# Kernel tuning notes

Measured on AMD Instinct MI355X. Metric: run time of the kernel, lower is better.

## Reference

```python
import jax, jax.numpy as jnp
import numpy as np

N_NODES = 100000
N_EDGES = 1600000
EMBED_DIM = 64


def setup_inputs() -> dict:
    key = jax.random.key(0)
    k_x, k_e, k_w, k_b = jax.random.split(key, 4)
    x = jax.random.normal(k_x, (N_NODES, EMBED_DIM), dtype=jnp.float32)
    edge_index = jax.random.randint(k_e, (2, N_EDGES), 0, N_NODES, dtype=jnp.int64)
    # nn.Linear(embed_dim, embed_dim): weight [out, in], bias [out]
    W = jax.random.normal(k_w, (EMBED_DIM, EMBED_DIM), dtype=jnp.float32) * (1.0 / np.sqrt(EMBED_DIM))
    b = jax.random.normal(k_b, (EMBED_DIM,), dtype=jnp.float32) * 0.01
    return {"x": x, "edge_index": edge_index, "W": W, "b": b, "num_node": N_NODES}


def reference(x, edge_index, W, b, num_node):
    source_nodes, target_nodes = edge_index[0], edge_index[1]
    # h = relu(Linear(x))  -> [N, d]
    h = jax.nn.relu(jnp.einsum("nd,od->no", x, W) + b)
    # gather messages at target nodes: [E, d]
    msgs = h[target_nodes]
    # scatter-add into source node slots (index_add_)
    aggr = jax.ops.segment_sum(msgs, source_nodes, num_segments=num_node)
    # mean normalization: bincount clamped to >= 1
    counts = jnp.bincount(source_nodes, length=num_node).astype(jnp.float32)
    counts = jnp.maximum(counts, 1.0)
    # dropout is identity at inference (training=False)
    return aggr / counts[:, None]
```

## Files before the change

### kernel.cpp

```cpp
#include <hip/hip_runtime.h>
#include <hip/hip_bf16.h>

#define DIM 64
#define SCAN_B 256

__global__ void detect_layout_kernel(const int* __restrict__ ei32,
                                     int* __restrict__ flag) {
  int v = ei32[2 * threadIdx.x + 1];
  unsigned long long m = __ballot(v != 0);
  if (threadIdx.x == 0) *flag = (m == 0ULL) ? 1 : 0;
}

__device__ __forceinline__ int load_idx(const int* ei32, int is64, size_t pos) {
  return is64 ? ei32[2 * pos] : ei32[pos];
}

__global__ __launch_bounds__(256) void hist_rank_kernel(
    const int* __restrict__ ei32, const int* __restrict__ flag,
    int* __restrict__ counts, int* __restrict__ rank, int E) {
  int e = blockIdx.x * 256 + threadIdx.x;
  if (e >= E) return;
  int src = load_idx(ei32, *flag, (size_t)e);
  rank[e] = atomicAdd(&counts[src], 1);
}

__global__ void scan1_kernel(const int* __restrict__ counts,
                             int* __restrict__ offsets,
                             int* __restrict__ partials, int N) {
  __shared__ int s[SCAN_B];
  int t = threadIdx.x;
  int i = blockIdx.x * SCAN_B + t;
  int v = (i < N) ? counts[i] : 0;
  s[t] = v;
  __syncthreads();
  for (int off = 1; off < SCAN_B; off <<= 1) {
    int add = (t >= off) ? s[t - off] : 0;
    __syncthreads();
    s[t] += add;
    __syncthreads();
  }
  if (i < N) offsets[i] = s[t] - v;
  if (t == SCAN_B - 1) partials[blockIdx.x] = s[t];
}

__global__ void scan2_kernel(int* __restrict__ partials, int nb) {
  __shared__ int s[512];
  int t = threadIdx.x;
  int v = (t < nb) ? partials[t] : 0;
  s[t] = v;
  __syncthreads();
  for (int off = 1; off < 512; off <<= 1) {
    int add = (t >= off) ? s[t - off] : 0;
    __syncthreads();
    s[t] += add;
    __syncthreads();
  }
  if (t < nb) partials[t] = s[t] - v;
}

__global__ void scan3_kernel(int* __restrict__ offsets,
                             const int* __restrict__ partials, int N) {
  int i = blockIdx.x * SCAN_B + threadIdx.x;
  if (i < N) offsets[i] += partials[blockIdx.x];
}

__global__ __launch_bounds__(256) void place_kernel(
    const int* __restrict__ ei32, const int* __restrict__ flag,
    const int* __restrict__ offsets, const int* __restrict__ rank,
    int* __restrict__ bucket, int E) {
  int e = blockIdx.x * 256 + threadIdx.x;
  if (e >= E) return;
  int is64 = *flag;
  int src = load_idx(ei32, is64, (size_t)e);
  int tgt = load_idx(ei32, is64, (size_t)E + e);
  __builtin_nontemporal_store(tgt, &bucket[offsets[src] + rank[e]]);
}

__global__ __launch_bounds__(256) void linear_relu_kernel(
    const float* __restrict__ x, const float* __restrict__ W,
    const float* __restrict__ b, float* __restrict__ h, int N) {
  __shared__ float Ws[DIM * DIM];
  __shared__ float bs[DIM];
  for (int i = threadIdx.x; i < DIM * DIM; i += 256) Ws[i] = W[i];
  if (threadIdx.x < DIM) bs[threadIdx.x] = b[threadIdx.x];
  __syncthreads();

  int row = blockIdx.x * 256 + threadIdx.x;
  if (row >= N) return;

  const float4* xr = (const float4*)(x + (size_t)row * DIM);
  float acc[DIM];
#pragma unroll
  for (int o = 0; o < DIM; ++o) acc[o] = bs[o];

#pragma unroll
  for (int i4 = 0; i4 < DIM / 4; ++i4) {
    float4 xv = xr[i4];
#pragma unroll
    for (int o = 0; o < DIM; ++o) {
      const float* wrow = &Ws[o * DIM + i4 * 4];
      acc[o] = fmaf(xv.x, wrow[0], acc[o]);
      acc[o] = fmaf(xv.y, wrow[1], acc[o]);
      acc[o] = fmaf(xv.z, wrow[2], acc[o]);
      acc[o] = fmaf(xv.w, wrow[3], acc[o]);
    }
  }

  float4* hr = (float4*)(h + (size_t)row * DIM);
#pragma unroll
  for (int o4 = 0; o4 < DIM / 4; ++o4) {
    float4 v;
    v.x = fmaxf(acc[o4 * 4 + 0], 0.0f);
    v.y = fmaxf(acc[o4 * 4 + 1], 0.0f);
    v.z = fmaxf(acc[o4 * 4 + 2], 0.0f);
    v.w = fmaxf(acc[o4 * 4 + 3], 0.0f);
    hr[o4] = v;
  }
}

__global__ __launch_bounds__(256) void gather_kernel(
    const float* __restrict__ h, const int* __restrict__ offsets,
    const int* __restrict__ counts, const int* __restrict__ bucket,
    float* __restrict__ out, int N) {
  int wid = (blockIdx.x * 256 + threadIdx.x) >> 6;
  int lane = threadIdx.x & 63;
  if (wid >= N) return;

  int deg = counts[wid];
  int start = offsets[wid];
  float a0 = 0.0f, a1 = 0.0f, a2 = 0.0f, a3 = 0.0f;

  for (int j0 = 0; j0 < deg; j0 += 64) {
    int m = min(deg - j0, 64);
    int t = (lane < m) ? __builtin_nontemporal_load(&bucket[start + j0 + lane])
                       : 0;
    int j = 0;
    for (; j + 4 <= m; j += 4) {
      int t0 = __shfl(t, j);
      int t1 = __shfl(t, j + 1);
      int t2 = __shfl(t, j + 2);
      int t3 = __shfl(t, j + 3);
      float v0 = h[(size_t)t0 * DIM + lane];
      float v1 = h[(size_t)t1 * DIM + lane];
      float v2 = h[(size_t)t2 * DIM + lane];
      float v3 = h[(size_t)t3 * DIM + lane];
      a0 += v0;
      a1 += v1;
      a2 += v2;
      a3 += v3;
    }
    for (; j < m; ++j) {
      int tj = __shfl(t, j);
      a0 += h[(size_t)tj * DIM + lane];
    }
  }

  float c = (float)max(deg, 1);
  float acc = (a0 + a1) + (a2 + a3);
  __builtin_nontemporal_store(acc / c, &out[(size_t)wid * DIM + lane]);
}

extern "C" void kernel_launch(void* const* d_in, const int* in_sizes, int n_in,
                              void* d_out, int out_size, void* d_ws, size_t ws_size,
                              hipStream_t stream) {
  const float* x = (const float*)d_in[0];
  const int* ei32 = (const int*)d_in[1];
  const float* W = (const float*)d_in[2];
  const float* b = (const float*)d_in[3];

  const int N = in_sizes[0] / DIM;
  const int E = in_sizes[1] / 2;

  float* out = (float*)d_out;

  char* p = (char*)d_ws;
  int* bucket = (int*)p;   p += (size_t)E * 4;
  int* counts = (int*)p;   p += (size_t)N * 4;
  int* offsets = (int*)p;  p += (size_t)N * 4;
  int* partials = (int*)p; p += 512 * 4;
  int* flag = (int*)p;     p += 16;
  p = (char*)(((uintptr_t)p + 15) & ~(uintptr_t)15);
  float* h = (float*)p;
  int* rank = (int*)p;

  const int nb1 = (N + SCAN_B - 1) / SCAN_B;
  const int eb = (E + 255) / 256;

  hipMemsetAsync(counts, 0, (size_t)N * 4, stream);

  detect_layout_kernel<<<1, 64, 0, stream>>>(ei32, flag);

  hist_rank_kernel<<<eb, 256, 0, stream>>>(ei32, flag, counts, rank, E);

  scan1_kernel<<<nb1, SCAN_B, 0, stream>>>(counts, offsets, partials, N);
  scan2_kernel<<<1, 512, 0, stream>>>(partials, nb1);
  scan3_kernel<<<nb1, SCAN_B, 0, stream>>>(offsets, partials, N);

  place_kernel<<<eb, 256, 0, stream>>>(ei32, flag, offsets, rank, bucket, E);

  linear_relu_kernel<<<(N + 255) / 256, 256, 0, stream>>>(x, W, b, h, N);

  gather_kernel<<<(N * 64 + 255) / 256, 256, 0, stream>>>(h, offsets, counts,
                                                          bucket, out, N);
}
```

Before: 330.0 us.

## Fuse linear-relu with histogram kernel and widen gather unroll to eight

Merges the linear+ReLU and the edge histogram/rank pass into one launch, using block-index ranges to split the work. Both can then run concurrently, and one kernel launch is removed. The rank array moves into the output buffer (which gather later overwrites) so it no longer aliases h, and its stores and loads become nontemporal. The gather loop now keeps eight independent loads in flight instead of four. The fused kernel reserves shared memory for every block, including the histogram blocks that never use it, which may lower occupancy for those blocks.

```diff
diff --git a/kernel.cpp b/kernel.cpp
--- a/kernel.cpp
+++ b/kernel.cpp
@@ -15,13 +15,59 @@
   return is64 ? ei32[2 * pos] : ei32[pos];
 }
 
-__global__ __launch_bounds__(256) void hist_rank_kernel(
+__global__ __launch_bounds__(256) void lin_hist_kernel(
+    const float* __restrict__ x, const float* __restrict__ W,
+    const float* __restrict__ b, float* __restrict__ h, int N, int nbLin,
     const int* __restrict__ ei32, const int* __restrict__ flag,
     int* __restrict__ counts, int* __restrict__ rank, int E) {
-  int e = blockIdx.x * 256 + threadIdx.x;
-  if (e >= E) return;
-  int src = load_idx(ei32, *flag, (size_t)e);
-  rank[e] = atomicAdd(&counts[src], 1);
+  __shared__ float Ws[DIM * DIM];
+  __shared__ float bs[DIM];
+
+  if (blockIdx.x >= nbLin) {
+    int e = (blockIdx.x - nbLin) * 256 + threadIdx.x;
+    if (e < E) {
+      int src = load_idx(ei32, *flag, (size_t)e);
+      int r = atomicAdd(&counts[src], 1);
+      __builtin_nontemporal_store(r, &rank[e]);
+    }
+    return;
+  }
+
+  for (int i = threadIdx.x; i < DIM * DIM; i += 256) Ws[i] = W[i];
+  if (threadIdx.x < DIM) bs[threadIdx.x] = b[threadIdx.x];
+  __syncthreads();
+
+  int row = blockIdx.x * 256 + threadIdx.x;
+  if (row >= N) return;
+
+  const float4* xr = (const float4*)(x + (size_t)row * DIM);
+  float acc[DIM];
+#pragma unroll
+  for (int o = 0; o < DIM; ++o) acc[o] = bs[o];
+
+#pragma unroll
+  for (int i4 = 0; i4 < DIM / 4; ++i4) {
+    float4 xv = xr[i4];
+#pragma unroll
+    for (int o = 0; o < DIM; ++o) {
+      const float* wrow = &Ws[o * DIM + i4 * 4];
+      acc[o] = fmaf(xv.x, wrow[0], acc[o]);
+      acc[o] = fmaf(xv.y, wrow[1], acc[o]);
+      acc[o] = fmaf(xv.z, wrow[2], acc[o]);
+      acc[o] = fmaf(xv.w, wrow[3], acc[o]);
+    }
+  }
+
+  float4* hr = (float4*)(h + (size_t)row * DIM);
+#pragma unroll
+  for (int o4 = 0; o4 < DIM / 4; ++o4) {
+    float4 v;
+    v.x = fmaxf(acc[o4 * 4 + 0], 0.0f);
+    v.y = fmaxf(acc[o4 * 4 + 1], 0.0f);
+    v.z = fmaxf(acc[o4 * 4 + 2], 0.0f);
+    v.w = fmaxf(acc[o4 * 4 + 3], 0.0f);
+    hr[o4] = v;
+  }
 }
 
 __global__ void scan1_kernel(const int* __restrict__ counts,
@@ -73,49 +119,8 @@
   int is64 = *flag;
   int src = load_idx(ei32, is64, (size_t)e);
   int tgt = load_idx(ei32, is64, (size_t)E + e);
-  __builtin_nontemporal_store(tgt, &bucket[offsets[src] + rank[e]]);
-}
-
-__global__ __launch_bounds__(256) void linear_relu_kernel(
-    const float* __restrict__ x, const float* __restrict__ W,
-    const float* __restrict__ b, float* __restrict__ h, int N) {
-  __shared__ float Ws[DIM * DIM];
-  __shared__ float bs[DIM];
-  for (int i = threadIdx.x; i < DIM * DIM; i += 256) Ws[i] = W[i];
-  if (threadIdx.x < DIM) bs[threadIdx.x] = b[threadIdx.x];
-  __syncthreads();
-
-  int row = blockIdx.x * 256 + threadIdx.x;
-  if (row >= N) return;
-
-  const float4* xr = (const float4*)(x + (size_t)row * DIM);
-  float acc[DIM];
-#pragma unroll
-  for (int o = 0; o < DIM; ++o) acc[o] = bs[o];
-
-#pragma unroll
-  for (int i4 = 0; i4 < DIM / 4; ++i4) {
-    float4 xv = xr[i4];
-#pragma unroll
-    for (int o = 0; o < DIM; ++o) {
-      const float* wrow = &Ws[o * DIM + i4 * 4];
-      acc[o] = fmaf(xv.x, wrow[0], acc[o]);
-      acc[o] = fmaf(xv.y, wrow[1], acc[o]);
-      acc[o] = fmaf(xv.z, wrow[2], acc[o]);
-      acc[o] = fmaf(xv.w, wrow[3], acc[o]);
-    }
-  }
-
-  float4* hr = (float4*)(h + (size_t)row * DIM);
-#pragma unroll
-  for (int o4 = 0; o4 < DIM / 4; ++o4) {
-    float4 v;
-    v.x = fmaxf(acc[o4 * 4 + 0], 0.0f);
-    v.y = fmaxf(acc[o4 * 4 + 1], 0.0f);
-    v.z = fmaxf(acc[o4 * 4 + 2], 0.0f);
-    v.w = fmaxf(acc[o4 * 4 + 3], 0.0f);
-    hr[o4] = v;
-  }
+  int r = __builtin_nontemporal_load(&rank[e]);
+  __builtin_nontemporal_store(tgt, &bucket[offsets[src] + r]);
 }
 
 __global__ __launch_bounds__(256) void gather_kernel(
@@ -128,26 +133,33 @@
 
   int deg = counts[wid];
   int start = offsets[wid];
-  float a0 = 0.0f, a1 = 0.0f, a2 = 0.0f, a3 = 0.0f;
+  float a0 = 0.f, a1 = 0.f, a2 = 0.f, a3 = 0.f;
+  float a4 = 0.f, a5 = 0.f, a6 = 0.f, a7 = 0.f;
 
   for (int j0 = 0; j0 < deg; j0 += 64) {
     int m = min(deg - j0, 64);
     int t = (lane < m) ? __builtin_nontemporal_load(&bucket[start + j0 + lane])
                        : 0;
     int j = 0;
-    for (; j + 4 <= m; j += 4) {
+    for (; j + 8 <= m; j += 8) {
       int t0 = __shfl(t, j);
       int t1 = __shfl(t, j + 1);
       int t2 = __shfl(t, j + 2);
       int t3 = __shfl(t, j + 3);
+      int t4 = __shfl(t, j + 4);
+      int t5 = __shfl(t, j + 5);
+      int t6 = __shfl(t, j + 6);
+      int t7 = __shfl(t, j + 7);
       float v0 = h[(size_t)t0 * DIM + lane];
       float v1 = h[(size_t)t1 * DIM + lane];
       float v2 = h[(size_t)t2 * DIM + lane];
       float v3 = h[(size_t)t3 * DIM + lane];
-      a0 += v0;
-      a1 += v1;
-      a2 += v2;
-      a3 += v3;
+      float v4 = h[(size_t)t4 * DIM + lane];
+      float v5 = h[(size_t)t5 * DIM + lane];
+      float v6 = h[(size_t)t6 * DIM + lane];
+      float v7 = h[(size_t)t7 * DIM + lane];
+      a0 += v0; a1 += v1; a2 += v2; a3 += v3;
+      a4 += v4; a5 += v5; a6 += v6; a7 += v7;
     }
     for (; j < m; ++j) {
       int tj = __shfl(t, j);
@@ -156,7 +168,7 @@
   }
 
   float c = (float)max(deg, 1);
-  float acc = (a0 + a1) + (a2 + a3);
+  float acc = ((a0 + a1) + (a2 + a3)) + ((a4 + a5) + (a6 + a7));
   __builtin_nontemporal_store(acc / c, &out[(size_t)wid * DIM + lane]);
 }
 
@@ -172,6 +184,8 @@
   const int E = in_sizes[1] / 2;
 
   float* out = (float*)d_out;
+
+  int* rank = (int*)d_out;
 
   char* p = (char*)d_ws;
   int* bucket = (int*)p;   p += (size_t)E * 4;
@@ -181,16 +195,17 @@
   int* flag = (int*)p;     p += 16;
   p = (char*)(((uintptr_t)p + 15) & ~(uintptr_t)15);
   float* h = (float*)p;
-  int* rank = (int*)p;
 
   const int nb1 = (N + SCAN_B - 1) / SCAN_B;
   const int eb = (E + 255) / 256;
+  const int nbLin = (N + 255) / 256;
 
   hipMemsetAsync(counts, 0, (size_t)N * 4, stream);
 
   detect_layout_kernel<<<1, 64, 0, stream>>>(ei32, flag);
 
-  hist_rank_kernel<<<eb, 256, 0, stream>>>(ei32, flag, counts, rank, E);
+  lin_hist_kernel<<<nbLin + eb, 256, 0, stream>>>(x, W, b, h, N, nbLin, ei32,
+                                                  flag, counts, rank, E);
 
   scan1_kernel<<<nb1, SCAN_B, 0, stream>>>(counts, offsets, partials, N);
   scan2_kernel<<<1, 512, 0, stream>>>(partials, nb1);
@@ -198,8 +213,6 @@
 
   place_kernel<<<eb, 256, 0, stream>>>(ei32, flag, offsets, rank, bucket, E);
 
-  linear_relu_kernel<<<(N + 255) / 256, 256, 0, stream>>>(x, W, b, h, N);
-
   gather_kernel<<<(N * 64 + 255) / 256, 256, 0, stream>>>(h, offsets, counts,
                                                           bucket, out, N);
 }
```

After: 308.2 us. 6.6% less time.
